# Optimization experiments

Measured on AMD Instinct MI355X. Metric: run time of the kernel, lower is better.

The kernel has to match this reference:

```python
import jax, jax.numpy as jnp
import numpy as np

BS, S, WIDTH, MODES = 2, 512, 64, 16
P = S * (S - 1) // 2
IU, JU = np.triu_indices(S, 1)  # upper-triangle (i<j) index constants
COLL_COEF = 0.9  # training=True path


def spectral_conv(x, w):
    # x: (bs, c_in, n), w: (c_in, c_out, modes, 2)
    n = x.shape[-1]
    xf = jnp.fft.rfft(x, axis=2, norm='ortho')  # (bs, c_in, n//2+1) complex
    wm = w[..., 0] + 1j * w[..., 1]
    out_m = jnp.einsum('bix,iox->box', xf[:, :, :MODES], wm)
    pad = jnp.zeros((x.shape[0], w.shape[1], n // 2 + 1 - MODES), dtype=out_m.dtype)
    return jnp.fft.irfft(jnp.concatenate([out_m, pad], axis=2), n=n, axis=2, norm='ortho')


def dsmc(x, a, rvec):
    # x, a: (bs, c, n); rvec: (bs, c, P) unit vectors along c.  dt=1, v = a*dt.
    bs, c, n = x.shape
    v = a
    x_r = jnp.linalg.norm(x[:, :, :, None] - x[:, :, None, :], axis=1)  # (bs, n, n)
    v_r = jnp.linalg.norm(v[:, :, :, None] - v[:, :, None, :], axis=1)
    v_cm = (v[:, :, :, None] + v[:, :, None, :]) * 0.5  # (bs, c, n, n)
    x_cm = (x[:, :, :, None] + x[:, :, None, :]) * 0.5
    u_x = jnp.exp(-x_r)
    v_r_max = jnp.max(v_r, axis=(1, 2), keepdims=True)  # (bs,1,1)
    mask = v_r / v_r_max * u_x
    cm = mask > (1.0 - COLL_COEF)  # collision mask (bs, n, n)
    # antisymmetric projection of v_r upper triangle onto random unit vectors
    proj = v_r[:, IU, JU][:, None, :] * rvec  # (bs, c, P)
    vrl = (jnp.zeros((bs, c, n, n), x.dtype)
           .at[:, :, IU, JU].set(proj)
           .at[:, :, JU, IU].set(-proj))
    delta_v = v_cm + vrl - v[:, :, :, None]
    cmf = cm.astype(x.dtype)
    v_new = v + jnp.sum(delta_v * cmf[:, None], axis=2)  # sum over partners i
    cmf = cmf + jnp.eye(n, dtype=x.dtype)[None]  # add self
    x_new = jnp.sum(x_cm * cmf[:, None], axis=2) / jnp.sum(cmf, axis=2)[:, None, :]
    x_new = x_new + v_new  # x = x + v*dt
    return x_new, v_new


def setup_inputs() -> dict:
    key = jax.random.key(0)
    ks = jax.random.split(key, 12)
    x = jax.random.normal(ks[0], (BS, S, 2), jnp.float32)
    v = jax.random.normal(ks[1], (BS, WIDTH, S), jnp.float32)
    vecs = jax.random.normal(ks[2], (4, BS, WIDTH, P), jnp.float32)
    vecs = vecs / jnp.linalg.norm(vecs, axis=2, keepdims=True)  # unit vectors over chnl
    fc0_w = jax.random.normal(ks[3], (2, WIDTH), jnp.float32) * 0.5
    fc0_b = jax.random.normal(ks[4], (WIDTH,), jnp.float32) * 0.1
    scale = 1.0 / (WIDTH * WIDTH)
    spec_w = jax.random.uniform(ks[5], (4, WIDTH, WIDTH, MODES, 2), jnp.float32) * scale
    conv_w = jax.random.normal(ks[6], (4, WIDTH, WIDTH), jnp.float32) * (WIDTH ** -0.5)
    conv_b = jax.random.normal(ks[7], (4, WIDTH), jnp.float32) * 0.05
    fc1_w = jax.random.normal(ks[8], (WIDTH, 128), jnp.float32) * (WIDTH ** -0.5)
    fc1_b = jnp.zeros((128,), jnp.float32)
    fc2_w = jax.random.normal(ks[9], (128, 1), jnp.float32) * (128 ** -0.5)
    fc2_b = jnp.zeros((1,), jnp.float32)
    return {"x": x, "v": v, "vecs": vecs, "fc0_w": fc0_w, "fc0_b": fc0_b,
            "spec_w": spec_w, "conv_w": conv_w, "conv_b": conv_b,
            "fc1_w": fc1_w, "fc1_b": fc1_b, "fc2_w": fc2_w, "fc2_b": fc2_b}


def reference(x, v, vecs, fc0_w, fc0_b, spec_w, conv_w, conv_b, fc1_w, fc1_b, fc2_w, fc2_b):
    # NOTE: v is overwritten by a*dt inside KINET_DSMC2 in the original; kept for signature fidelity.
    h = x @ fc0_w + fc0_b          # (bs, s, width)
    h = jnp.transpose(h, (0, 2, 1))  # (bs, width, s)
    for i in range(4):
        a = spectral_conv(h, spec_w[i])
        p = jnp.einsum('oi,bin->bon', conv_w[i], h) + conv_b[i][None, :, None]
        h, vv = dsmc(p, a, vecs[i])
        if i < 3:
            h = jax.nn.relu(h)
    h = jnp.transpose(h, (0, 2, 1))  # (bs, s, width)
    h = jax.nn.relu(h @ fc1_w + fc1_b)
    return h @ fc2_w + fc2_b  # (bs, s, 1)
```

## Files before the change

### kernel.cpp

```cpp
#include <hip/hip_runtime.h>
#include <math.h>

#define S 512
#define W 64
#define MODES 16
#define PAIRS 130816
#define INV_SQRT_N 0.04419417382415922f
#define TWO_PI_OVER_N 0.012271846303085130f

__global__ __launch_bounds__(256) void k_fft(const float* __restrict__ h,
                                             const float* __restrict__ x,
                                             const float* __restrict__ fc0w,
                                             const float* __restrict__ fc0b,
                                             float* __restrict__ Xf, int first) {
    int b = blockIdx.x >> 6, ch = blockIdx.x & 63;
    int tid = threadIdx.x;
    float v0, v1;
    if (first) {
        float w0 = fc0w[ch], w1 = fc0w[64 + ch], bb = fc0b[ch];
        const float* xb = x + (size_t)b * S * 2;
        v0 = xb[2 * tid] * w0 + xb[2 * tid + 1] * w1 + bb;
        v1 = xb[2 * (tid + 256)] * w0 + xb[2 * (tid + 256) + 1] * w1 + bb;
    } else {
        const float* hp = h + (b * W + ch) * S;
        v0 = hp[tid]; v1 = hp[tid + 256];
    }
    float c1, s1;
    sincosf(TWO_PI_OVER_N * (float)tid, &s1, &c1);
    float cm = 1.f, sm = 0.f;
    float ap = v0 + v1, am = v0 - v1;
    float re[MODES], im[MODES];
#pragma unroll
    for (int m = 0; m < MODES; ++m) {
        float a = (m & 1) ? am : ap;
        re[m] = a * cm;
        im[m] = -a * sm;
        float nc = cm * c1 - sm * s1;
        float ns = sm * c1 + cm * s1;
        cm = nc; sm = ns;
    }
    __shared__ float part[4][32];
    int lane = tid & 63, wv = tid >> 6;
#pragma unroll
    for (int m = 0; m < MODES; ++m) {
        float r = re[m], ii = im[m];
        for (int off = 32; off; off >>= 1) {
            r += __shfl_down(r, off);
            ii += __shfl_down(ii, off);
        }
        if (lane == 0) { part[wv][2 * m] = r; part[wv][2 * m + 1] = ii; }
    }
    __syncthreads();
    if (tid < 32) {
        float s = part[0][tid] + part[1][tid] + part[2][tid] + part[3][tid];
        Xf[(b * W + ch) * 32 + tid] = s * INV_SQRT_N;
    }
}

__global__ __launch_bounds__(256) void k_mix(const float* __restrict__ Xf,
                                             const float* __restrict__ specw,
                                             float* __restrict__ Y, int l) {
    int b = blockIdx.x >> 6, o = blockIdx.x & 63;
    int tid = threadIdx.x, m = tid & 15, ip = tid >> 4;
    __shared__ float Xs[2048];
    for (int idx = tid; idx < 2048; idx += 256) Xs[idx] = Xf[b * 2048 + idx];
    __syncthreads();
    float ar = 0.f, ai = 0.f;
#pragma unroll
    for (int q = 0; q < 4; ++q) {
        int i = ip * 4 + q;
        const float* wp = specw + (size_t)(((l * W + i) * W + o) * MODES + m) * 2;
        float wr = wp[0], wi = wp[1];
        float xr = Xs[i * 32 + 2 * m], xi = Xs[i * 32 + 2 * m + 1];
        ar += xr * wr - xi * wi;
        ai += xr * wi + xi * wr;
    }
    __shared__ float redr[16][17], redi[16][17];
    redr[ip][m] = ar; redi[ip][m] = ai;
    __syncthreads();
    if (tid < 16) {
        float sr = 0.f, si = 0.f;
        for (int p = 0; p < 16; ++p) { sr += redr[p][tid]; si += redi[p][tid]; }
        Y[(b * W + o) * 32 + 2 * tid] = sr;
        Y[(b * W + o) * 32 + 2 * tid + 1] = si;
    }
}

__global__ __launch_bounds__(256) void k_ac(const float* __restrict__ Y,
                                            const float* __restrict__ h,
                                            const float* __restrict__ x,
                                            const float* __restrict__ fc0w,
                                            const float* __restrict__ fc0b,
                                            const float* __restrict__ convw,
                                            const float* __restrict__ convb,
                                            float* __restrict__ aT,
                                            float* __restrict__ pT,
                                            unsigned* __restrict__ vmax,
                                            int l, int first) {
    int blk = blockIdx.x;
    int b = blk >> 7, t0 = (blk & 127) * 4;
    int tid = threadIdx.x;
    int o = tid & 63, tg = tid >> 6;
    if (blk == 0 && tid < 2) vmax[tid] = 0u;
    __shared__ float hs[64 * 5];
    {
        int r = tid >> 2, t = tid & 3;
        if (first) {
            const float* xb = x + ((size_t)b * S + t0 + t) * 2;
            hs[r * 5 + t] = xb[0] * fc0w[r] + xb[1] * fc0w[64 + r] + fc0b[r];
        } else {
            hs[r * 5 + t] = h[(b * W + r) * S + t0 + t];
        }
    }
    float yr[MODES], yi[MODES];
    const float4* yp = (const float4*)(Y + b * 2048 + o * 32);
#pragma unroll
    for (int q = 0; q < 8; ++q) {
        float4 y4 = yp[q];
        yr[2 * q] = y4.x; yi[2 * q] = y4.y;
        yr[2 * q + 1] = y4.z; yi[2 * q + 1] = y4.w;
    }
    int t = t0 + tg;
    float c1, s1;
    sincosf(TWO_PI_OVER_N * (float)t, &s1, &c1);
    float cm = c1, sm = s1;
    float acc = yr[0];
#pragma unroll
    for (int m = 1; m < MODES; ++m) {
        acc += 2.0f * (yr[m] * cm - yi[m] * sm);
        float nc = cm * c1 - sm * s1;
        float ns = sm * c1 + cm * s1;
        cm = nc; sm = ns;
    }
    aT[((size_t)b * S + t) * W + o] = acc * INV_SQRT_N;
    __syncthreads();
    float pacc = convb[l * W + o];
    const float4* wp = (const float4*)(convw + l * 4096 + o * 64);
#pragma unroll
    for (int i4 = 0; i4 < 16; ++i4) {
        float4 w4 = wp[i4];
        pacc = fmaf(w4.x, hs[(4 * i4 + 0) * 5 + tg], pacc);
        pacc = fmaf(w4.y, hs[(4 * i4 + 1) * 5 + tg], pacc);
        pacc = fmaf(w4.z, hs[(4 * i4 + 2) * 5 + tg], pacc);
        pacc = fmaf(w4.w, hs[(4 * i4 + 3) * 5 + tg], pacc);
    }
    pT[((size_t)b * S + t) * W + o] = pacc;
}

__global__ __launch_bounds__(256) void k_pair(const float* __restrict__ pT,
                                              const float* __restrict__ aT,
                                              float* __restrict__ vr,
                                              float* __restrict__ uxm,
                                              unsigned* __restrict__ vmax) {
    int blk = blockIdx.x;
    int b = blk >> 8;
    int rest = blk & 255;
    int i0 = (rest & 15) * 32, j0 = (rest >> 4) * 32;
    int tid = threadIdx.x;
    int tx = tid & 15, ty = tid >> 4;
    __shared__ __align__(16) float Pi[64 * 34];
    __shared__ __align__(16) float Pj[64 * 34];
    __shared__ __align__(16) float Vi[64 * 34];
    __shared__ __align__(16) float Vj[64 * 34];
    for (int idx = tid; idx < 2048; idx += 256) {
        int k = idx >> 6, c = idx & 63;
        Pi[c * 34 + k] = pT[(b * S + i0 + k) * W + c];
        Pj[c * 34 + k] = pT[(b * S + j0 + k) * W + c];
        Vi[c * 34 + k] = aT[(b * S + i0 + k) * W + c];
        Vj[c * 34 + k] = aT[(b * S + j0 + k) * W + c];
    }
    __syncthreads();
    float ax[2][2] = {{0.f, 0.f}, {0.f, 0.f}};
    float av[2][2] = {{0.f, 0.f}, {0.f, 0.f}};
    for (int c = 0; c < W; ++c) {
        float2 pi = *(const float2*)&Pi[c * 34 + 2 * tx];
        float2 pj = *(const float2*)&Pj[c * 34 + 2 * ty];
        float2 vi = *(const float2*)&Vi[c * 34 + 2 * tx];
        float2 vj = *(const float2*)&Vj[c * 34 + 2 * ty];
        float d;
        d = pi.x - pj.x; ax[0][0] = fmaf(d, d, ax[0][0]);
        d = pi.y - pj.x; ax[1][0] = fmaf(d, d, ax[1][0]);
        d = pi.x - pj.y; ax[0][1] = fmaf(d, d, ax[0][1]);
        d = pi.y - pj.y; ax[1][1] = fmaf(d, d, ax[1][1]);
        d = vi.x - vj.x; av[0][0] = fmaf(d, d, av[0][0]);
        d = vi.y - vj.x; av[1][0] = fmaf(d, d, av[1][0]);
        d = vi.x - vj.y; av[0][1] = fmaf(d, d, av[0][1]);
        d = vi.y - vj.y; av[1][1] = fmaf(d, d, av[1][1]);
    }
    float mx = 0.f;
#pragma unroll
    for (int jj = 0; jj < 2; ++jj) {
#pragma unroll
        for (int ii = 0; ii < 2; ++ii) {
            int i = i0 + 2 * tx + ii, j = j0 + 2 * ty + jj;
            float xr = sqrtf(ax[ii][jj]);
            float vv = sqrtf(av[ii][jj]);
            vr[((size_t)b * S + j) * S + i] = vv;
            uxm[((size_t)b * S + j) * S + i] = expf(-xr);
            mx = fmaxf(mx, vv);
        }
    }
    __shared__ float mxs[4];
    for (int off = 32; off; off >>= 1) mx = fmaxf(mx, __shfl_xor(mx, off));
    if ((tid & 63) == 0) mxs[tid >> 6] = mx;
    __syncthreads();
    if (tid == 0) {
        float m = fmaxf(fmaxf(mxs[0], mxs[1]), fmaxf(mxs[2], mxs[3]));
        atomicMax(&vmax[b], __float_as_uint(m));
    }
}

__global__ __launch_bounds__(256) void k_mpf(const float* __restrict__ vr,
                                             const float* __restrict__ uxm,
                                             const unsigned* __restrict__ vmaxu,
                                             const float* __restrict__ aT,
                                             const float* __restrict__ pT,
                                             const float* __restrict__ vecs,
                                             float* __restrict__ h_std,
                                             const float* __restrict__ fc1w,
                                             const float* __restrict__ fc1b,
                                             const float* __restrict__ fc2w,
                                             const float* __restrict__ fc2b,
                                             float* __restrict__ out,
                                             int l, int do_relu, int do_head) {
    int b = blockIdx.x >> 9, q = blockIdx.x & 511;
    int tid = threadIdx.x, lane = tid & 63, wv = tid >> 6;
    __shared__ float wrow[S];
    __shared__ float SV[4][64], SX[4][64], TP[4][64];
    __shared__ float hrow[64];
    __shared__ int cnt4[4];
    const float* vrp = vr + ((size_t)b * S + q) * S;
    const float* uxp = uxm + ((size_t)b * S + q) * S;
    float vmax = __uint_as_float(vmaxu[b]);
    int mycnt = 0;
    {
        float2 v2 = *(const float2*)&vrp[2 * tid];
        float2 u2 = *(const float2*)&uxp[2 * tid];
        bool a0 = (v2.x / vmax) * u2.x > 0.1f;
        bool a1 = (v2.y / vmax) * u2.y > 0.1f;
        wrow[2 * tid] = a0 ? v2.x : 0.f;
        wrow[2 * tid + 1] = a1 ? v2.y : 0.f;
        mycnt = (a0 ? 1 : 0) + (a1 ? 1 : 0);
    }
    for (int o = 32; o; o >>= 1) mycnt += __shfl_down(mycnt, o);
    if (lane == 0) cnt4[wv] = mycnt;
    __syncthreads();
    float A = (float)(cnt4[0] + cnt4[1] + cnt4[2] + cnt4[3]);
    float svp = 0.f, sxp = 0.f, tp = 0.f;
    const float* aTb = aT + (size_t)b * S * W;
    const float* pTb = pT + (size_t)b * S * W;
    const float* Rb = vecs + (size_t)((l * 2 + b) * W + lane) * PAIRS;
    int triq = q * 511 - ((q * (q - 1)) >> 1);
    for (int k = 0; k < 128; ++k) {
        int p = (wv << 7) + k;
        float w = wrow[p];
        if (w != 0.f) {
            svp += aTb[p * W + lane];
            sxp += pTb[p * W + lane];
            int idx; float sgn;
            if (p < q) { idx = p * 511 - ((p * (p - 1)) >> 1) + (q - p - 1); sgn = 1.f; }
            else       { idx = triq + (p - q - 1); sgn = -1.f; }
            tp = fmaf(sgn * w, Rb[idx], tp);
        }
    }
    SV[wv][lane] = svp; SX[wv][lane] = sxp; TP[wv][lane] = tp;
    __syncthreads();
    if (wv == 0) {
        float sv = SV[0][lane] + SV[1][lane] + SV[2][lane] + SV[3][lane];
        float sx = SX[0][lane] + SX[1][lane] + SX[2][lane] + SX[3][lane];
        float T  = TP[0][lane] + TP[1][lane] + TP[2][lane] + TP[3][lane];
        float vj = aTb[q * W + lane], xj = pTb[q * W + lane];
        float vnew = vj + 0.5f * (A * vj - sv) + T;
        float accx = 0.5f * (A * xj + sx);
        float xnew = (xj + accx) / (A + 1.0f) + vnew;
        if (do_relu) xnew = fmaxf(xnew, 0.0f);
        if (!do_head) h_std[((size_t)b * W + lane) * S + q] = xnew;
        else hrow[lane] = xnew;
    }
    if (do_head) {
        __syncthreads();
        if (wv == 0) {
            float a0 = fc1b[lane], a1 = fc1b[lane + 64];
            for (int cc = 0; cc < W; ++cc) {
                float hv = hrow[cc];
                a0 = fmaf(hv, fc1w[cc * 128 + lane], a0);
                a1 = fmaf(hv, fc1w[cc * 128 + lane + 64], a1);
            }
            a0 = fmaxf(a0, 0.f); a1 = fmaxf(a1, 0.f);
            float p = a0 * fc2w[lane] + a1 * fc2w[lane + 64];
            for (int off = 32; off; off >>= 1) p += __shfl_down(p, off);
            if (lane == 0) out[b * S + q] = p + fc2b[0];
        }
    }
}

extern "C" void kernel_launch(void* const* d_in, const int* in_sizes, int n_in,
                              void* d_out, int out_size, void* d_ws, size_t ws_size,
                              hipStream_t stream) {
    const float* x = (const float*)d_in[0];
    const float* vecs = (const float*)d_in[2];
    const float* fc0w = (const float*)d_in[3];
    const float* fc0b = (const float*)d_in[4];
    const float* specw = (const float*)d_in[5];
    const float* convw = (const float*)d_in[6];
    const float* convb = (const float*)d_in[7];
    const float* fc1w = (const float*)d_in[8];
    const float* fc1b = (const float*)d_in[9];
    const float* fc2w = (const float*)d_in[10];
    const float* fc2b = (const float*)d_in[11];
    float* out = (float*)d_out;

    char* ws = (char*)d_ws;
    unsigned* vmax = (unsigned*)ws;
    float* h_std = (float*)(ws + 256);
    float* aT = h_std + 65536;
    float* pT = aT + 65536;
    float* Xf = pT + 65536;
    float* Yb = Xf + 4096;
    float* vrbuf = Yb + 4096;
    float* uxbuf = vrbuf + 524288;

    for (int l = 0; l < 4; ++l) {
        int first = (l == 0) ? 1 : 0;
        k_fft<<<128, 256, 0, stream>>>(h_std, x, fc0w, fc0b, Xf, first);
        k_mix<<<128, 256, 0, stream>>>(Xf, specw, Yb, l);
        k_ac<<<256, 256, 0, stream>>>(Yb, h_std, x, fc0w, fc0b, convw, convb,
                                      aT, pT, vmax, l, first);
        k_pair<<<512, 256, 0, stream>>>(pT, aT, vrbuf, uxbuf, vmax);
        k_mpf<<<1024, 256, 0, stream>>>(vrbuf, uxbuf, vmax, aT, pT, vecs,
                                        h_std, fc1w, fc1b, fc2w, fc2b, out,
                                        l, (l < 3) ? 1 : 0, (l == 3) ? 1 : 0);
    }
}
```

Baseline: 651.4 us.

## Fuse spectral mix, inverse transform and pointwise conv into pairwise kernel

Merges the mode-mixing, inverse-DFT/conv and pairwise-distance kernels into one kernel, so each pair tile recomputes its own a and p rows in shared memory instead of reading them from global buffers. The spectral weights are transposed once up front for coalesced access, and the vmax reset moves into the FFT kernel. Two launches per layer go away, but the mixing and per-row transform are now computed redundantly by every tile (16x), so there is more arithmetic per block and more shared memory use.

```diff
diff --git a/kernel.cpp b/kernel.cpp
--- a/kernel.cpp
+++ b/kernel.cpp
@@ -8,13 +8,28 @@
 #define INV_SQRT_N 0.04419417382415922f
 #define TWO_PI_OVER_N 0.012271846303085130f
 
+__global__ __launch_bounds__(256) void k_prep(const float* __restrict__ specw,
+                                              float* __restrict__ wmT) {
+    int bi = blockIdx.x;
+    int tid = threadIdx.x, o = tid & 63, tg = tid >> 6;
+#pragma unroll
+    for (int k = 0; k < 4; ++k) {
+        int m = tg * 4 + k;
+        float2 wv = *(const float2*)(specw + (((size_t)bi * 64 + o) * 16 + m) * 2);
+        *(float2*)(wmT + (((size_t)bi * 16 + m) * 64 + o) * 2) = wv;
+    }
+}
+
 __global__ __launch_bounds__(256) void k_fft(const float* __restrict__ h,
                                              const float* __restrict__ x,
                                              const float* __restrict__ fc0w,
                                              const float* __restrict__ fc0b,
-                                             float* __restrict__ Xf, int first) {
+                                             float* __restrict__ Xf,
+                                             unsigned* __restrict__ vmax,
+                                             int first) {
     int b = blockIdx.x >> 6, ch = blockIdx.x & 63;
     int tid = threadIdx.x;
+    if (blockIdx.x == 0 && tid < 2) vmax[tid] = 0u;
     float v0, v1;
     if (first) {
         float w0 = fc0w[ch], w1 = fc0w[64 + ch], bb = fc0b[ch];
@@ -57,121 +72,114 @@
     }
 }
 
-__global__ __launch_bounds__(256) void k_mix(const float* __restrict__ Xf,
-                                             const float* __restrict__ specw,
-                                             float* __restrict__ Y, int l) {
-    int b = blockIdx.x >> 6, o = blockIdx.x & 63;
-    int tid = threadIdx.x, m = tid & 15, ip = tid >> 4;
-    __shared__ float Xs[2048];
-    for (int idx = tid; idx < 2048; idx += 256) Xs[idx] = Xf[b * 2048 + idx];
-    __syncthreads();
-    float ar = 0.f, ai = 0.f;
-#pragma unroll
-    for (int q = 0; q < 4; ++q) {
-        int i = ip * 4 + q;
-        const float* wp = specw + (size_t)(((l * W + i) * W + o) * MODES + m) * 2;
-        float wr = wp[0], wi = wp[1];
-        float xr = Xs[i * 32 + 2 * m], xi = Xs[i * 32 + 2 * m + 1];
-        ar += xr * wr - xi * wi;
-        ai += xr * wi + xi * wr;
-    }
-    __shared__ float redr[16][17], redi[16][17];
-    redr[ip][m] = ar; redi[ip][m] = ai;
-    __syncthreads();
-    if (tid < 16) {
-        float sr = 0.f, si = 0.f;
-        for (int p = 0; p < 16; ++p) { sr += redr[p][tid]; si += redi[p][tid]; }
-        Y[(b * W + o) * 32 + 2 * tid] = sr;
-        Y[(b * W + o) * 32 + 2 * tid + 1] = si;
-    }
-}
-
-__global__ __launch_bounds__(256) void k_ac(const float* __restrict__ Y,
-                                            const float* __restrict__ h,
-                                            const float* __restrict__ x,
-                                            const float* __restrict__ fc0w,
-                                            const float* __restrict__ fc0b,
-                                            const float* __restrict__ convw,
-                                            const float* __restrict__ convb,
-                                            float* __restrict__ aT,
-                                            float* __restrict__ pT,
-                                            unsigned* __restrict__ vmax,
-                                            int l, int first) {
-    int blk = blockIdx.x;
-    int b = blk >> 7, t0 = (blk & 127) * 4;
-    int tid = threadIdx.x;
-    int o = tid & 63, tg = tid >> 6;
-    if (blk == 0 && tid < 2) vmax[tid] = 0u;
-    __shared__ float hs[64 * 5];
-    {
-        int r = tid >> 2, t = tid & 3;
-        if (first) {
-            const float* xb = x + ((size_t)b * S + t0 + t) * 2;
-            hs[r * 5 + t] = xb[0] * fc0w[r] + xb[1] * fc0w[64 + r] + fc0b[r];
-        } else {
-            hs[r * 5 + t] = h[(b * W + r) * S + t0 + t];
-        }
-    }
-    float yr[MODES], yi[MODES];
-    const float4* yp = (const float4*)(Y + b * 2048 + o * 32);
-#pragma unroll
-    for (int q = 0; q < 8; ++q) {
-        float4 y4 = yp[q];
-        yr[2 * q] = y4.x; yi[2 * q] = y4.y;
-        yr[2 * q + 1] = y4.z; yi[2 * q + 1] = y4.w;
-    }
-    int t = t0 + tg;
-    float c1, s1;
-    sincosf(TWO_PI_OVER_N * (float)t, &s1, &c1);
-    float cm = c1, sm = s1;
-    float acc = yr[0];
-#pragma unroll
-    for (int m = 1; m < MODES; ++m) {
-        acc += 2.0f * (yr[m] * cm - yi[m] * sm);
-        float nc = cm * c1 - sm * s1;
-        float ns = sm * c1 + cm * s1;
-        cm = nc; sm = ns;
-    }
-    aT[((size_t)b * S + t) * W + o] = acc * INV_SQRT_N;
-    __syncthreads();
-    float pacc = convb[l * W + o];
-    const float4* wp = (const float4*)(convw + l * 4096 + o * 64);
-#pragma unroll
-    for (int i4 = 0; i4 < 16; ++i4) {
-        float4 w4 = wp[i4];
-        pacc = fmaf(w4.x, hs[(4 * i4 + 0) * 5 + tg], pacc);
-        pacc = fmaf(w4.y, hs[(4 * i4 + 1) * 5 + tg], pacc);
-        pacc = fmaf(w4.z, hs[(4 * i4 + 2) * 5 + tg], pacc);
-        pacc = fmaf(w4.w, hs[(4 * i4 + 3) * 5 + tg], pacc);
-    }
-    pT[((size_t)b * S + t) * W + o] = pacc;
-}
-
-__global__ __launch_bounds__(256) void k_pair(const float* __restrict__ pT,
-                                              const float* __restrict__ aT,
-                                              float* __restrict__ vr,
-                                              float* __restrict__ uxm,
-                                              unsigned* __restrict__ vmax) {
+__global__ __launch_bounds__(256) void k_map(const float* __restrict__ Xf,
+                                             const float* __restrict__ wmT,
+                                             const float* __restrict__ h,
+                                             const float* __restrict__ x,
+                                             const float* __restrict__ fc0w,
+                                             const float* __restrict__ fc0b,
+                                             const float* __restrict__ convw,
+                                             const float* __restrict__ convb,
+                                             float* __restrict__ aT,
+                                             float* __restrict__ pT,
+                                             float* __restrict__ vr,
+                                             float* __restrict__ uxm,
+                                             unsigned* __restrict__ vmax,
+                                             int l, int first) {
     int blk = blockIdx.x;
     int b = blk >> 8;
     int rest = blk & 255;
     int i0 = (rest & 15) * 32, j0 = (rest >> 4) * 32;
     int tid = threadIdx.x;
+    int o = tid & 63, og = tid >> 6;
+    __shared__ __align__(16) float Ys[64 * 34];
+    __shared__ __align__(16) float hs[64][64];
+    __shared__ __align__(16) float PV[4 * 64 * 34];
+    float* Pi = PV;
+    float* Pj = PV + 2176;
+    float* Vi = PV + 4352;
+    float* Vj = PV + 6528;
+    float* Xs = PV;
+    for (int idx = tid; idx < 2048; idx += 256) Xs[idx] = Xf[b * 2048 + idx];
+    for (int idx = tid; idx < 4096; idx += 256) {
+        int c = idx >> 6, r = idx & 63;
+        int tr = (r < 32) ? (i0 + r) : (j0 + r - 32);
+        if (first) {
+            const float* xb = x + ((size_t)b * S + tr) * 2;
+            hs[c][r] = xb[0] * fc0w[c] + xb[1] * fc0w[64 + c] + fc0b[c];
+        } else {
+            hs[c][r] = h[(b * W + c) * S + tr];
+        }
+    }
+    __syncthreads();
+    {
+        float ar[4] = {0.f, 0.f, 0.f, 0.f}, ai[4] = {0.f, 0.f, 0.f, 0.f};
+        const float2* wp = (const float2*)wmT + ((size_t)(l * 1024) + og * 4) * 64 + o;
+        for (int i = 0; i < 64; ++i) {
+#pragma unroll
+            for (int mm = 0; mm < 4; ++mm) {
+                float2 wv = wp[(size_t)(i * 16 + mm) * 64];
+                float2 xv = *(const float2*)&Xs[i * 32 + (og * 4 + mm) * 2];
+                ar[mm] += xv.x * wv.x - xv.y * wv.y;
+                ai[mm] += xv.x * wv.y + xv.y * wv.x;
+            }
+        }
+#pragma unroll
+        for (int mm = 0; mm < 4; ++mm) {
+            float2 yv; yv.x = ar[mm]; yv.y = ai[mm];
+            *(float2*)&Ys[o * 34 + (og * 4 + mm) * 2] = yv;
+        }
+    }
+    __syncthreads();
+    {
+        float yr[MODES], yi[MODES];
+#pragma unroll
+        for (int m = 0; m < MODES; ++m) {
+            float2 yv = *(const float2*)&Ys[o * 34 + 2 * m];
+            yr[m] = yv.x; yi[m] = yv.y;
+        }
+        float4 wreg[16];
+        const float4* wp4 = (const float4*)(convw + l * 4096 + o * 64);
+#pragma unroll
+        for (int q = 0; q < 16; ++q) wreg[q] = wp4[q];
+        float bias = convb[l * W + o];
+        bool diag = (i0 == j0);
+        for (int k = 0; k < 16; ++k) {
+            int r = og + 4 * k;
+            int tr = (r < 32) ? (i0 + r) : (j0 + r - 32);
+            float c1, s1;
+            sincosf(TWO_PI_OVER_N * (float)tr, &s1, &c1);
+            float cm = c1, sm = s1;
+            float acc = yr[0];
+#pragma unroll
+            for (int m = 1; m < MODES; ++m) {
+                acc += 2.0f * (yr[m] * cm - yi[m] * sm);
+                float nc = cm * c1 - sm * s1;
+                float ns = sm * c1 + cm * s1;
+                cm = nc; sm = ns;
+            }
+            float av = acc * INV_SQRT_N;
+            float pv = bias;
+#pragma unroll
+            for (int q = 0; q < 16; ++q) {
+                float4 w4 = wreg[q];
+                pv = fmaf(w4.x, hs[4 * q + 0][r], pv);
+                pv = fmaf(w4.y, hs[4 * q + 1][r], pv);
+                pv = fmaf(w4.z, hs[4 * q + 2][r], pv);
+                pv = fmaf(w4.w, hs[4 * q + 3][r], pv);
+            }
+            if (r < 32) { Pi[o * 34 + r] = pv; Vi[o * 34 + r] = av; }
+            else        { Pj[o * 34 + (r - 32)] = pv; Vj[o * 34 + (r - 32)] = av; }
+            if (diag && r < 32) {
+                aT[((size_t)b * S + tr) * W + o] = av;
+                pT[((size_t)b * S + tr) * W + o] = pv;
+            }
+        }
+    }
+    __syncthreads();
     int tx = tid & 15, ty = tid >> 4;
-    __shared__ __align__(16) float Pi[64 * 34];
-    __shared__ __align__(16) float Pj[64 * 34];
-    __shared__ __align__(16) float Vi[64 * 34];
-    __shared__ __align__(16) float Vj[64 * 34];
-    for (int idx = tid; idx < 2048; idx += 256) {
-        int k = idx >> 6, c = idx & 63;
-        Pi[c * 34 + k] = pT[(b * S + i0 + k) * W + c];
-        Pj[c * 34 + k] = pT[(b * S + j0 + k) * W + c];
-        Vi[c * 34 + k] = aT[(b * S + i0 + k) * W + c];
-        Vj[c * 34 + k] = aT[(b * S + j0 + k) * W + c];
-    }
-    __syncthreads();
     float ax[2][2] = {{0.f, 0.f}, {0.f, 0.f}};
-    float av[2][2] = {{0.f, 0.f}, {0.f, 0.f}};
+    float av2[2][2] = {{0.f, 0.f}, {0.f, 0.f}};
     for (int c = 0; c < W; ++c) {
         float2 pi = *(const float2*)&Pi[c * 34 + 2 * tx];
         float2 pj = *(const float2*)&Pj[c * 34 + 2 * ty];
@@ -182,10 +190,10 @@
         d = pi.y - pj.x; ax[1][0] = fmaf(d, d, ax[1][0]);
         d = pi.x - pj.y; ax[0][1] = fmaf(d, d, ax[0][1]);
         d = pi.y - pj.y; ax[1][1] = fmaf(d, d, ax[1][1]);
-        d = vi.x - vj.x; av[0][0] = fmaf(d, d, av[0][0]);
-        d = vi.y - vj.x; av[1][0] = fmaf(d, d, av[1][0]);
-        d = vi.x - vj.y; av[0][1] = fmaf(d, d, av[0][1]);
-        d = vi.y - vj.y; av[1][1] = fmaf(d, d, av[1][1]);
+        d = vi.x - vj.x; av2[0][0] = fmaf(d, d, av2[0][0]);
+        d = vi.y - vj.x; av2[1][0] = fmaf(d, d, av2[1][0]);
+        d = vi.x - vj.y; av2[0][1] = fmaf(d, d, av2[0][1]);
+        d = vi.y - vj.y; av2[1][1] = fmaf(d, d, av2[1][1]);
     }
     float mx = 0.f;
 #pragma unroll
@@ -194,7 +202,7 @@
         for (int ii = 0; ii < 2; ++ii) {
             int i = i0 + 2 * tx + ii, j = j0 + 2 * ty + jj;
             float xr = sqrtf(ax[ii][jj]);
-            float vv = sqrtf(av[ii][jj]);
+            float vv = sqrtf(av2[ii][jj]);
             vr[((size_t)b * S + j) * S + i] = vv;
             uxm[((size_t)b * S + j) * S + i] = expf(-xr);
             mx = fmaxf(mx, vv);
@@ -316,17 +324,17 @@
     float* aT = h_std + 65536;
     float* pT = aT + 65536;
     float* Xf = pT + 65536;
-    float* Yb = Xf + 4096;
-    float* vrbuf = Yb + 4096;
+    float* wmT = Xf + 4096;
+    float* vrbuf = wmT + 524288;
     float* uxbuf = vrbuf + 524288;
 
+    k_prep<<<256, 256, 0, stream>>>(specw, wmT);
     for (int l = 0; l < 4; ++l) {
         int first = (l == 0) ? 1 : 0;
-        k_fft<<<128, 256, 0, stream>>>(h_std, x, fc0w, fc0b, Xf, first);
-        k_mix<<<128, 256, 0, stream>>>(Xf, specw, Yb, l);
-        k_ac<<<256, 256, 0, stream>>>(Yb, h_std, x, fc0w, fc0b, convw, convb,
-                                      aT, pT, vmax, l, first);
-        k_pair<<<512, 256, 0, stream>>>(pT, aT, vrbuf, uxbuf, vmax);
+        k_fft<<<128, 256, 0, stream>>>(h_std, x, fc0w, fc0b, Xf, vmax, first);
+        k_map<<<512, 256, 0, stream>>>(Xf, wmT, h_std, x, fc0w, fc0b,
+                                       convw, convb, aT, pT, vrbuf, uxbuf,
+                                       vmax, l, first);
         k_mpf<<<1024, 256, 0, stream>>>(vrbuf, uxbuf, vmax, aT, pT, vecs,
                                         h_std, fc1w, fc1b, fc2w, fc2b, out,
                                         l, (l < 3) ? 1 : 0, (l == 3) ? 1 : 0);
```

Result: slower. 739.1 us (+13.5%).
